# Optimization experiments

Hardware: AMD Instinct MI355X
Metric: run time of the kernel (lower is better)

The kernel has to match this reference:

```python
import jax, jax.numpy as jnp
import numpy as np

EPS = 1e-6      # torch F.pairwise_distance default eps (added to the difference)
MARGIN = 1.0

def _cdist_eps(a, b):
    # Exact ||a_i - b_j + eps||_2 via expansion:
    # ||a-b+eps||^2 = ||a||^2 + ||b||^2 - 2 a.b + 2*eps*(sum(a)-sum(b)) + D*eps^2
    D = a.shape[-1]
    sq = (jnp.sum(a * a, axis=1)[:, None]
          + jnp.sum(b * b, axis=1)[None, :]
          - 2.0 * (a @ b.T)
          + 2.0 * EPS * (jnp.sum(a, axis=1)[:, None] - jnp.sum(b, axis=1)[None, :])
          + D * EPS * EPS)
    return jnp.sqrt(jnp.maximum(sq, 0.0))

def setup_inputs() -> dict:
    key = jax.random.key(0)
    k1, k2, k3 = jax.random.split(key, 3)
    B, D = 4096, 1024
    return {
        'anchor_embeddings': jax.random.normal(k1, (B, D), dtype=jnp.float32),
        'positive_embeddings': jax.random.normal(k2, (B, D), dtype=jnp.float32),
        'negative_embeddings': jax.random.normal(k3, (B, D), dtype=jnp.float32),
    }

def reference(anchor_embeddings, positive_embeddings, negative_embeddings):
    a, p, n = anchor_embeddings, positive_embeddings, negative_embeddings
    # per-row anchor-positive and anchor-negative distances
    d_ap = jnp.linalg.norm(a - p + EPS, axis=-1)          # [B]
    d_an_row = jnp.linalg.norm(a - n + EPS, axis=-1)      # [B]

    # hardest negative: for each anchor, max over negatives with dist < d_ap[i], else 0
    dan_mat = _cdist_eps(a, n)                            # [B, B]
    mask_n = dan_mat < d_ap[:, None]
    hard_n = jnp.where(mask_n.any(axis=1),
                       jnp.max(jnp.where(mask_n, dan_mat, -jnp.inf), axis=1),
                       0.0)
    d_an = jnp.mean(hard_n)                               # scalar

    # hardest positive: for each anchor, min over positives with dist > d(a_i, n_i), else 0
    dpp_mat = _cdist_eps(a, p)                            # [B, B]
    mask_p = dpp_mat > d_an_row[:, None]
    hard_p = jnp.where(mask_p.any(axis=1),
                       jnp.min(jnp.where(mask_p, dpp_mat, jnp.inf), axis=1),
                       0.0)
    d_pp = jnp.mean(hard_p)                               # scalar

    loss = jnp.mean(jnp.clip(d_ap - 0.5 * d_pp - 0.5 * d_an + MARGIN, 0.0, None))
    return loss
```

## Files before the change

kernel.cpp:

```cpp
#include <hip/hip_runtime.h>


#define NB 4096
#define DIM 1024
#define EPSF 1e-6f
#define D_EPS2 (1024.0f * 1e-6f * 1e-6f)

#define BM 128
#define BK 64

typedef __bf16  bf16x8 __attribute__((ext_vector_type(8)));
typedef float   f32x4  __attribute__((ext_vector_type(4)));

__device__ __forceinline__ unsigned short f2bf(float x) {
    unsigned u = __float_as_uint(x);
    u += 0x7FFFu + ((u >> 16) & 1u);
    return (unsigned short)(u >> 16);
}

__device__ __forceinline__ void g2l16(const unsigned short* g, unsigned short* l) {
    __builtin_amdgcn_global_load_lds(
        (const __attribute__((address_space(1))) unsigned int*)g,
        (__attribute__((address_space(3))) unsigned int*)l, 16, 0, 0);
}


__global__ __launch_bounds__(256) void row_stats_kernel(
    const float* __restrict__ a, const float* __restrict__ p,
    const float* __restrict__ n,
    unsigned short* __restrict__ abf, unsigned short* __restrict__ pbf,
    unsigned short* __restrict__ nbf, float* __restrict__ stats)
{
    const int t    = threadIdx.x;
    const int wave = t >> 6, lane = t & 63;
    const int row  = blockIdx.x * 4 + wave;
    const size_t base = (size_t)row * DIM;

    const float4* a4 = (const float4*)(a + base);
    const float4* p4 = (const float4*)(p + base);
    const float4* n4 = (const float4*)(n + base);

    float v[8] = {0,0,0,0,0,0,0,0};
#pragma unroll
    for (int c = 0; c < 4; c++) {
        const int idx = c * 64 + lane;
        const float4 va = a4[idx];
        const float4 vp = p4[idx];
        const float4 vn = n4[idx];
        const float fa[4] = {va.x, va.y, va.z, va.w};
        const float fp[4] = {vp.x, vp.y, vp.z, vp.w};
        const float fn[4] = {vn.x, vn.y, vn.z, vn.w};
#pragma unroll
        for (int e = 0; e < 4; e++) {
            v[0] += fa[e];           v[1] += fa[e] * fa[e];
            v[2] += fp[e];           v[3] += fp[e] * fp[e];
            v[4] += fn[e];           v[5] += fn[e] * fn[e];
            float dp = fa[e] - fp[e] + EPSF;  v[6] += dp * dp;
            float dn = fa[e] - fn[e] + EPSF;  v[7] += dn * dn;
        }
        ushort4 ba, bp, bn;
        ba.x = f2bf(fa[0]); ba.y = f2bf(fa[1]); ba.z = f2bf(fa[2]); ba.w = f2bf(fa[3]);
        bp.x = f2bf(fp[0]); bp.y = f2bf(fp[1]); bp.z = f2bf(fp[2]); bp.w = f2bf(fp[3]);
        bn.x = f2bf(fn[0]); bn.y = f2bf(fn[1]); bn.z = f2bf(fn[2]); bn.w = f2bf(fn[3]);
        ((ushort4*)(abf + base))[idx] = ba;
        ((ushort4*)(pbf + base))[idx] = bp;
        ((ushort4*)(nbf + base))[idx] = bn;
    }

#pragma unroll
    for (int m = 32; m >= 1; m >>= 1)
#pragma unroll
        for (int q = 0; q < 8; q++) v[q] += __shfl_xor(v[q], m);

    if (lane == 0) {
        stats[0 * NB + row] = v[1] + 2.0f * EPSF * v[0] + D_EPS2;
        stats[1 * NB + row] = v[5] - 2.0f * EPSF * v[4];
        stats[2 * NB + row] = v[3] - 2.0f * EPSF * v[2];
        stats[3 * NB + row] = sqrtf(v[6]);
        stats[4 * NB + row] = sqrtf(v[7]);
        ((unsigned*)stats)[5 * NB + row] = 0u;
        ((unsigned*)stats)[6 * NB + row] = 0x7f800000u;
    }
}

__global__ __launch_bounds__(256, 3) void gemm_mask_kernel(
    const unsigned short* __restrict__ Abf,
    const unsigned short* __restrict__ Nbf,
    const unsigned short* __restrict__ Pbf,
    float* __restrict__ stats)
{
    const int flat = (int)blockIdx.x;
    const int swz  = (flat & 7) * 256 + (flat >> 3);
    const int bz   = swz >> 10;
    const int rem  = swz & 1023;
    const int i0   = (rem & 31) * BM;
    const int j0   = (rem >> 5) * BM;

    const unsigned short* __restrict__ Bbf = bz ? Pbf : Nbf;

    __shared__ unsigned short sA[BM * BK];
    __shared__ unsigned short sB[BM * BK];

    const int t    = threadIdx.x;
    const int wave = t >> 6, lane = t & 63;
    const int wm   = wave >> 1, wn = wave & 1;
    const int quad = lane >> 4, lrow = lane & 15;

    const int srow = lane >> 3;
    const int kch  = ((lane & 7) ^ srow) * 8;
    const unsigned short* gA = Abf + (size_t)(i0 + wave * 32 + srow) * DIM + kch;
    const unsigned short* gB = Bbf + (size_t)(j0 + wave * 32 + srow) * DIM + kch;
    unsigned short* lA = sA + (wave * 32) * BK;
    unsigned short* lB = sB + (wave * 32) * BK;

    const int rsw0 = ((0 * 4 + quad) ^ (lrow & 7)) * 8;
    const int rsw1 = ((1 * 4 + quad) ^ (lrow & 7)) * 8;
    const unsigned short* pa = sA + (wm * 64 + lrow) * BK;
    const unsigned short* pb = sB + (wn * 64 + lrow) * BK;

    f32x4 acc[4][4];
#pragma unroll
    for (int im = 0; im < 4; im++)
#pragma unroll
        for (int jn = 0; jn < 4; jn++)
            acc[im][jn] = (f32x4)(0.0f);

    for (int kt = 0; kt < DIM; kt += BK) {
        __syncthreads();
#pragma unroll
        for (int g = 0; g < 4; g++) {
            g2l16(gA + (size_t)kt + g * 8 * DIM, lA + g * 8 * BK);
            g2l16(gB + (size_t)kt + g * 8 * DIM, lB + g * 8 * BK);
        }
        __syncthreads();

#pragma unroll
        for (int half = 0; half < 2; half++) {
            const int rsw = half ? rsw1 : rsw0;
            bf16x8 afr[4], bfr[4];
#pragma unroll
            for (int im = 0; im < 4; im++)
                afr[im] = *(const bf16x8*)(pa + im * 16 * BK + rsw);
#pragma unroll
            for (int jn = 0; jn < 4; jn++)
                bfr[jn] = *(const bf16x8*)(pb + jn * 16 * BK + rsw);
#pragma unroll
            for (int im = 0; im < 4; im++)
#pragma unroll
                for (int jn = 0; jn < 4; jn++)
                    acc[im][jn] = __builtin_amdgcn_mfma_f32_16x16x32_bf16(
                        afr[im], bfr[jn], acc[im][jn], 0, 0, 0);
        }
    }

    const float* __restrict__ base_a = stats + 0 * NB;
    const float* __restrict__ cv     = stats + (bz ? 2 : 1) * NB;
    const float* __restrict__ cut_v  = stats + (bz ? 4 : 3) * NB;
    unsigned* __restrict__ hard = ((unsigned*)stats) + (bz ? 6 : 5) * NB;

#pragma unroll
    for (int im = 0; im < 4; im++) {
#pragma unroll
        for (int r = 0; r < 4; r++) {
            const int gi = i0 + wm * 64 + im * 16 + quad * 4 + r;
            const float cut = cut_v[gi];
            const float bi  = base_a[gi];
            if (bz == 0) {
                float best = 0.0f;
#pragma unroll
                for (int jn = 0; jn < 4; jn++) {
                    const int gj = j0 + wn * 64 + jn * 16 + lrow;
                    const float d = sqrtf(fmaxf(bi + cv[gj] - 2.0f * acc[im][jn][r], 0.0f));
                    if (d < cut && d > best) best = d;
                }
#pragma unroll
                for (int m = 1; m < 16; m <<= 1)
                    best = fmaxf(best, __shfl_xor(best, m));
                if (lrow == 0) {
                    const unsigned b_ = __float_as_uint(best);
                    if (b_ != 0u) atomicMax(hard + gi, b_);
                }
            } else {
                float best = __uint_as_float(0x7f800000u);
#pragma unroll
                for (int jn = 0; jn < 4; jn++) {
                    const int gj = j0 + wn * 64 + jn * 16 + lrow;
                    const float d = sqrtf(fmaxf(bi + cv[gj] - 2.0f * acc[im][jn][r], 0.0f));
                    if (d > cut && d < best) best = d;
                }
#pragma unroll
                for (int m = 1; m < 16; m <<= 1)
                    best = fminf(best, __shfl_xor(best, m));
                if (lrow == 0) {
                    const unsigned b_ = __float_as_uint(best);
                    if (b_ != 0x7f800000u) atomicMin(hard + gi, b_);
                }
            }
        }
    }
}

__global__ __launch_bounds__(1024) void finalize_kernel(
    const float* __restrict__ stats, float* __restrict__ out)
{
    const unsigned* hard_n = ((const unsigned*)stats) + 5 * NB;
    const unsigned* hard_p = ((const unsigned*)stats) + 6 * NB;
    const float*    d_ap   = stats + 3 * NB;
    const int t = threadIdx.x;
    const int wave = t >> 6, lane = t & 63;
    __shared__ float pn[16], pp[16];
    __shared__ float s_dan, s_dpp;

    float sn = 0.0f, sp = 0.0f;
    for (int i = t; i < NB; i += 1024) {
        sn += __uint_as_float(hard_n[i]);
        const unsigned hp = hard_p[i];
        if (hp != 0x7f800000u) sp += __uint_as_float(hp);
    }
#pragma unroll
    for (int m = 32; m >= 1; m >>= 1) {
        sn += __shfl_xor(sn, m);
        sp += __shfl_xor(sp, m);
    }
    if (lane == 0) { pn[wave] = sn; pp[wave] = sp; }
    __syncthreads();
    if (t == 0) {
        float an = 0.0f, ap = 0.0f;
#pragma unroll
        for (int w = 0; w < 16; w++) { an += pn[w]; ap += pp[w]; }
        s_dan = an / (float)NB;
        s_dpp = ap / (float)NB;
    }
    __syncthreads();
    const float dan = s_dan, dpp = s_dpp;

    float accv = 0.0f;
    for (int i = t; i < NB; i += 1024)
        accv += fmaxf(d_ap[i] - 0.5f * dpp - 0.5f * dan + 1.0f, 0.0f);
#pragma unroll
    for (int m = 32; m >= 1; m >>= 1) accv += __shfl_xor(accv, m);
    if (lane == 0) pn[wave] = accv;
    __syncthreads();
    if (t == 0) {
        float s = 0.0f;
#pragma unroll
        for (int w = 0; w < 16; w++) s += pn[w];
        out[0] = s / (float)NB;
    }
}

extern "C" void kernel_launch(void* const* d_in, const int* in_sizes, int n_in,
                              void* d_out, int out_size, void* d_ws, size_t ws_size,
                              hipStream_t stream) {
    const float* a = (const float*)d_in[0];
    const float* p = (const float*)d_in[1];
    const float* n = (const float*)d_in[2];
    float* out = (float*)d_out;

    unsigned short* abf = (unsigned short*)d_ws;
    unsigned short* pbf = abf + (size_t)NB * DIM;
    unsigned short* nbf = pbf + (size_t)NB * DIM;
    float* stats = (float*)(nbf + (size_t)NB * DIM);

    row_stats_kernel<<<NB / 4, 256, 0, stream>>>(a, p, n, abf, pbf, nbf, stats);

    gemm_mask_kernel<<<2048, 256, 0, stream>>>(abf, nbf, pbf, stats);

    finalize_kernel<<<1, 1024, 0, stream>>>(stats, out);
}
```

Before: 185.9 us.

## Use 256x256 tiles with double-buffered LDS and interleaved async loads in GEMM

The distance GEMM now uses 256x256 output tiles per 512-thread block, with 8 waves each computing 128x64, instead of 128x128 tiles per 256-thread block. The shared-memory stages are double-buffered and split into two K halves, so global-to-LDS loads for the next step are issued between MFMA groups, with explicit vmcnt waits and raw barriers replacing full __syncthreads. MFMA sections also raise wave priority via s_setprio. This is meant to raise arithmetic intensity and hide load latency, at the cost of more registers (32 accumulators per lane), only 512 blocks (two per CU), and fragile hand-managed synchronization.

```diff
diff --git a/kernel.cpp b/kernel.cpp
--- a/kernel.cpp
+++ b/kernel.cpp
@@ -6,8 +6,8 @@
 #define EPSF 1e-6f
 #define D_EPS2 (1024.0f * 1e-6f * 1e-6f)
 
-#define BM 128
-#define BK 64
+#define BT 256
+#define KHALF 32
 
 typedef __bf16  bf16x8 __attribute__((ext_vector_type(8)));
 typedef float   f32x4  __attribute__((ext_vector_type(4)));
@@ -83,75 +83,134 @@
     }
 }
 
-__global__ __launch_bounds__(256, 3) void gemm_mask_kernel(
+__global__ __launch_bounds__(512, 2) void gemm_mask_kernel(
     const unsigned short* __restrict__ Abf,
     const unsigned short* __restrict__ Nbf,
     const unsigned short* __restrict__ Pbf,
     float* __restrict__ stats)
 {
     const int flat = (int)blockIdx.x;
-    const int swz  = (flat & 7) * 256 + (flat >> 3);
-    const int bz   = swz >> 10;
-    const int rem  = swz & 1023;
-    const int i0   = (rem & 31) * BM;
-    const int j0   = (rem >> 5) * BM;
+    const int swz  = (flat & 7) * 64 + (flat >> 3);
+    const int bz   = swz >> 8;
+    const int rem  = swz & 255;
+    const int i0   = (rem & 15) * BT;
+    const int j0   = (rem >> 4) * BT;
 
     const unsigned short* __restrict__ Bbf = bz ? Pbf : Nbf;
 
-    __shared__ unsigned short sA[BM * BK];
-    __shared__ unsigned short sB[BM * BK];
+    __shared__ unsigned short sA[2][2][BT * KHALF];
+    __shared__ unsigned short sB[2][2][BT * KHALF];
 
     const int t    = threadIdx.x;
     const int wave = t >> 6, lane = t & 63;
-    const int wm   = wave >> 1, wn = wave & 1;
+    const int wr   = wave >> 2, wc = wave & 3;
     const int quad = lane >> 4, lrow = lane & 15;
 
-    const int srow = lane >> 3;
-    const int kch  = ((lane & 7) ^ srow) * 8;
-    const unsigned short* gA = Abf + (size_t)(i0 + wave * 32 + srow) * DIM + kch;
-    const unsigned short* gB = Bbf + (size_t)(j0 + wave * 32 + srow) * DIM + kch;
-    unsigned short* lA = sA + (wave * 32) * BK;
-    unsigned short* lB = sB + (wave * 32) * BK;
-
-    const int rsw0 = ((0 * 4 + quad) ^ (lrow & 7)) * 8;
-    const int rsw1 = ((1 * 4 + quad) ^ (lrow & 7)) * 8;
-    const unsigned short* pa = sA + (wm * 64 + lrow) * BK;
-    const unsigned short* pb = sB + (wn * 64 + lrow) * BK;
-
-    f32x4 acc[4][4];
-#pragma unroll
-    for (int im = 0; im < 4; im++)
+    const int srow = t >> 2;
+    const int gch  = ((t & 3) ^ ((srow >> 1) & 3)) * 8;
+    const unsigned short* gA = Abf + (size_t)(i0 + srow) * DIM + gch;
+    const unsigned short* gB = Bbf + (size_t)(j0 + srow) * DIM + gch;
+    const int lbase = wave * 512;
+
+    const int rsw  = (quad ^ ((lrow >> 1) & 3)) * 8;
+    const int arow = wr * 128 + lrow;
+    const int brow = wc * 64 + lrow;
+
+    f32x4 acc[8][4];
+#pragma unroll
+    for (int im = 0; im < 8; im++)
 #pragma unroll
         for (int jn = 0; jn < 4; jn++)
             acc[im][jn] = (f32x4)(0.0f);
 
-    for (int kt = 0; kt < DIM; kt += BK) {
-        __syncthreads();
-#pragma unroll
-        for (int g = 0; g < 4; g++) {
-            g2l16(gA + (size_t)kt + g * 8 * DIM, lA + g * 8 * BK);
-            g2l16(gB + (size_t)kt + g * 8 * DIM, lB + g * 8 * BK);
-        }
-        __syncthreads();
-
-#pragma unroll
-        for (int half = 0; half < 2; half++) {
-            const int rsw = half ? rsw1 : rsw0;
-            bf16x8 afr[4], bfr[4];
-#pragma unroll
-            for (int im = 0; im < 4; im++)
-                afr[im] = *(const bf16x8*)(pa + im * 16 * BK + rsw);
-#pragma unroll
-            for (int jn = 0; jn < 4; jn++)
-                bfr[jn] = *(const bf16x8*)(pb + jn * 16 * BK + rsw);
-#pragma unroll
-            for (int im = 0; im < 4; im++)
-#pragma unroll
-                for (int jn = 0; jn < 4; jn++)
-                    acc[im][jn] = __builtin_amdgcn_mfma_f32_16x16x32_bf16(
-                        afr[im], bfr[jn], acc[im][jn], 0, 0, 0);
-        }
-    }
+#define STG_A(NBUF, KS, KT)                                                   \
+    g2l16(gA + (size_t)(KT) + (KS) * KHALF,            &sA[NBUF][KS][lbase]); \
+    g2l16(gA + (size_t)(KT) + (KS) * KHALF + (size_t)128 * DIM,               \
+          &sA[NBUF][KS][4096 + lbase]);
+
+#define STG_B(NBUF, KS, KT)                                                   \
+    g2l16(gB + (size_t)(KT) + (KS) * KHALF,            &sB[NBUF][KS][lbase]); \
+    g2l16(gB + (size_t)(KT) + (KS) * KHALF + (size_t)128 * DIM,               \
+          &sB[NBUF][KS][4096 + lbase]);
+
+#define LDA4(DST, BUF, KS, IMB)                                               \
+    _Pragma("unroll")                                                         \
+    for (int m = 0; m < 4; m++)                                               \
+        DST[m] = *(const bf16x8*)&sA[BUF][KS][(arow + ((IMB) + m) * 16) * KHALF + rsw];
+
+#define LDB4(DST, BUF, KS)                                                    \
+    _Pragma("unroll")                                                         \
+    for (int j = 0; j < 4; j++)                                               \
+        DST[j] = *(const bf16x8*)&sB[BUF][KS][(brow + j * 16) * KHALF + rsw];
+
+#define MM16(IMB, AF, BF)                                                     \
+    __builtin_amdgcn_s_setprio(1);                                            \
+    _Pragma("unroll")                                                         \
+    for (int m = 0; m < 4; m++)                                               \
+        _Pragma("unroll")                                                     \
+        for (int j = 0; j < 4; j++)                                           \
+            acc[(IMB) + m][j] = __builtin_amdgcn_mfma_f32_16x16x32_bf16(      \
+                AF[m], BF[j], acc[(IMB) + m][j], 0, 0, 0);                    \
+    __builtin_amdgcn_s_setprio(0);
+
+#define BAR()     __builtin_amdgcn_s_barrier()
+#define VMCNT(N)  asm volatile("s_waitcnt vmcnt(" #N ")" ::: "memory")
+
+    STG_A(0, 0, 0);
+    STG_B(0, 0, 0);
+    STG_A(0, 1, 0);
+    STG_B(0, 1, 0);
+    VMCNT(4);
+    BAR();
+
+#pragma unroll 1
+    for (int kt15 = 0; kt15 < 15; ++kt15) {
+        const int cur = kt15 & 1, nxt = cur ^ 1;
+        const int kn  = (kt15 + 1) * 2 * KHALF;
+        bf16x8 af[4], bf[4];
+        LDA4(af, cur, 0, 0);
+        LDB4(bf, cur, 0);
+        STG_A(nxt, 0, kn);
+        MM16(0, af, bf);
+        LDA4(af, cur, 0, 4);
+        STG_B(nxt, 0, kn);
+        MM16(4, af, bf);
+        VMCNT(4);
+        BAR();
+        LDA4(af, cur, 1, 0);
+        LDB4(bf, cur, 1);
+        STG_A(nxt, 1, kn);
+        MM16(0, af, bf);
+        LDA4(af, cur, 1, 4);
+        STG_B(nxt, 1, kn);
+        MM16(4, af, bf);
+        VMCNT(4);
+        BAR();
+    }
+
+    {
+        bf16x8 af[4], bf[4];
+        LDA4(af, 1, 0, 0);
+        LDB4(bf, 1, 0);
+        MM16(0, af, bf);
+        LDA4(af, 1, 0, 4);
+        MM16(4, af, bf);
+        VMCNT(0);
+        BAR();
+        LDA4(af, 1, 1, 0);
+        LDB4(bf, 1, 1);
+        MM16(0, af, bf);
+        LDA4(af, 1, 1, 4);
+        MM16(4, af, bf);
+    }
+
+#undef BAR
+#undef VMCNT
+#undef MM16
+#undef LDB4
+#undef LDA4
+#undef STG_B
+#undef STG_A
 
     const float* __restrict__ base_a = stats + 0 * NB;
     const float* __restrict__ cv     = stats + (bz ? 2 : 1) * NB;
@@ -159,17 +218,17 @@
     unsigned* __restrict__ hard = ((unsigned*)stats) + (bz ? 6 : 5) * NB;
 
 #pragma unroll
-    for (int im = 0; im < 4; im++) {
+    for (int im = 0; im < 8; im++) {
 #pragma unroll
         for (int r = 0; r < 4; r++) {
-            const int gi = i0 + wm * 64 + im * 16 + quad * 4 + r;
+            const int gi = i0 + wr * 128 + im * 16 + quad * 4 + r;
             const float cut = cut_v[gi];
             const float bi  = base_a[gi];
             if (bz == 0) {
                 float best = 0.0f;
 #pragma unroll
                 for (int jn = 0; jn < 4; jn++) {
-                    const int gj = j0 + wn * 64 + jn * 16 + lrow;
+                    const int gj = j0 + wc * 64 + jn * 16 + lrow;
                     const float d = sqrtf(fmaxf(bi + cv[gj] - 2.0f * acc[im][jn][r], 0.0f));
                     if (d < cut && d > best) best = d;
                 }
@@ -184,7 +243,7 @@
                 float best = __uint_as_float(0x7f800000u);
 #pragma unroll
                 for (int jn = 0; jn < 4; jn++) {
-                    const int gj = j0 + wn * 64 + jn * 16 + lrow;
+                    const int gj = j0 + wc * 64 + jn * 16 + lrow;
                     const float d = sqrtf(fmaxf(bi + cv[gj] - 2.0f * acc[im][jn][r], 0.0f));
                     if (d > cut && d < best) best = d;
                 }
@@ -264,7 +323,7 @@
 
     row_stats_kernel<<<NB / 4, 256, 0, stream>>>(a, p, n, abf, pbf, nbf, stats);
 
-    gemm_mask_kernel<<<2048, 256, 0, stream>>>(abf, nbf, pbf, stats);
+    gemm_mask_kernel<<<512, 512, 0, stream>>>(abf, nbf, pbf, stats);
 
     finalize_kernel<<<1, 1024, 0, stream>>>(stats, out);
 }
```

Result: slower. 197.9 us (+6.4%).
